# Kernel optimization log

Measured on AMD Instinct MI355X. Metric: run time of the kernel, lower is better.

The kernel has to match this reference:

```python
import math
import jax, jax.numpy as jnp
import numpy as np
from jax import lax

DT = 0.1
IMG_W = 1920.0
IMG_H = 1080.0
DIAG = math.sqrt(IMG_W ** 2 + IMG_H ** 2)


def setup_inputs() -> dict:
    key = jax.random.key(0)
    k1, k2, k3, k4 = jax.random.split(key, 4)
    B, T = 524288, 64
    return {
        "speed": jax.random.uniform(k1, (B, T), dtype=jnp.float32),          # softplus-like, positive
        "yaw_rate": jax.random.normal(k2, (B, T), dtype=jnp.float32) * 0.05,  # rad/step
        "init_pos": jax.random.uniform(k3, (B, 2), dtype=jnp.float32),        # normalized x,y
        "init_heading": jax.random.normal(k4, (B,), dtype=jnp.float32),       # rad
    }


def reference(speed, yaw_rate, init_pos, init_heading):
    B, T = speed.shape
    dtype = speed.dtype
    # per-step yaw decay 0.97**t (the torch loop recomputes this every step; same values)
    decay = jnp.power(jnp.asarray(0.97, dtype), jnp.arange(T, dtype=dtype))
    v_seq = (speed * DIAG).T                      # (T, B) pixel-space speed
    w_seq = (yaw_rate * decay[None, :]).T         # (T, B) decayed yaw rate

    x0 = init_pos[:, 0] * IMG_W
    y0 = init_pos[:, 1] * IMG_H
    psi0 = init_heading

    def step(carry, inp):
        x, y, psi = carry
        v_t, w_t = inp
        is_straight = (jnp.abs(w_t) < 0.01).astype(dtype)
        sin_psi, cos_psi = jnp.sin(psi), jnp.cos(psi)
        dx_straight = v_t * cos_psi * DT
        dy_straight = v_t * sin_psi * DT
        w_safe = w_t + is_straight * 0.0001
        radius = v_t / w_safe
        psi_new = psi + w_t * DT
        dx_turn = radius * (jnp.sin(psi_new) - sin_psi)
        dy_turn = -radius * (jnp.cos(psi_new) - cos_psi)
        dx = is_straight * dx_straight + (1.0 - is_straight) * dx_turn
        dy = is_straight * dy_straight + (1.0 - is_straight) * dy_turn
        x = x + dx
        y = y + dy
        out = jnp.stack([x / IMG_W, y / IMG_H], axis=-1)  # (B, 2)
        return (x, y, psi_new), out

    _, pos = lax.scan(step, (x0, y0, psi0), (v_seq, w_seq))  # pos: (T, B, 2)
    return jnp.transpose(pos, (1, 0, 2))                     # (B, T, 2)
```

## Files before the change

kernel.cpp:

```cpp
#include <hip/hip_runtime.h>
#include <math.h>


#define T_STEPS 64

__global__ __launch_bounds__(256) void kin_scan_kernel(
    const float* __restrict__ speed,
    const float* __restrict__ yaw,
    const float* __restrict__ init_pos,
    const float* __restrict__ init_heading,
    float* __restrict__ out,
    int B)
{
    const float DT    = 0.1f;
    const float IMG_W = 1920.0f;
    const float IMG_H = 1080.0f;
    const float DIAG  = 2202.9071700822459f;
    const float INV_W = 1.0f / 1920.0f;
    const float INV_H = 1.0f / 1080.0f;
    const float LOG2_097 = -0.0439433475875970f;

    const int tid = blockIdx.x * blockDim.x + threadIdx.x;
    const int row = tid >> 4;
    if (row >= B) return;
    const int seg = tid & 15;
    const int t0  = seg * 4;

    const float4* sp4 = reinterpret_cast<const float4*>(speed) + (size_t)row * 16 + seg;
    const float4* yw4 = reinterpret_cast<const float4*>(yaw)   + (size_t)row * 16 + seg;
    float4 v4 = *sp4;
    float4 w4 = *yw4;

    float d  = exp2f((float)t0 * LOG2_097);
    float w0 = w4.x * d; d *= 0.97f;
    float w1 = w4.y * d; d *= 0.97f;
    float w2 = w4.z * d; d *= 0.97f;
    float w3 = w4.w * d;

    float wl = ((w0 + w1) + w2) + w3;
    float s  = wl;
    #pragma unroll
    for (int dlt = 1; dlt < 16; dlt <<= 1) {
        float o = __shfl_up(s, (unsigned)dlt, 16);
        if (seg >= dlt) s += o;
    }
    float wexcl = s - wl;

    const float psi0 = init_heading[row];
    const float2 ip  = reinterpret_cast<const float2*>(init_pos)[row];
    const float x0   = ip.x * IMG_W;
    const float y0   = ip.y * IMG_H;

    float p = psi0 + DT * wexcl;
    float sp, cp;
    sincosf(p, &sp, &cp);

    float dx[4], dy[4];
    float wv[4] = {w0, w1, w2, w3};
    float vv[4] = {v4.x * DIAG, v4.y * DIAG, v4.z * DIAG, v4.w * DIAG};
    #pragma unroll
    for (int j = 0; j < 4; ++j) {
        float v  = vv[j];
        float w  = wv[j];
        float th = w * DT;
        float t2 = th * th;
        float sd  = th * (1.0f + t2 * (-1.666666667e-1f + t2 * 8.333333333e-3f));
        float cm1 = t2 * (-0.5f + t2 * 4.166666667e-2f);
        float ds  = sp * cm1 + cp * sd;
        float dc  = cp * cm1 - sp * sd;
        bool  is_str = fabsf(w) < 0.01f;
        float w_safe = is_str ? (w + 1e-4f) : w;
        float r   = v / w_safe;
        float dxs = v * cp * DT;
        float dys = v * sp * DT;
        float dxt = r * ds;
        float dyt = -r * dc;
        dx[j] = is_str ? dxs : dxt;
        dy[j] = is_str ? dys : dyt;
        sp += ds;
        cp += dc;
    }

    float xi0 = dx[0];
    float xi1 = xi0 + dx[1];
    float xi2 = xi1 + dx[2];
    float xi3 = xi2 + dx[3];
    float yi0 = dy[0];
    float yi1 = yi0 + dy[1];
    float yi2 = yi1 + dy[2];
    float yi3 = yi2 + dy[3];

    float xs = xi3, ys = yi3;
    #pragma unroll
    for (int dlt = 1; dlt < 16; dlt <<= 1) {
        float ox = __shfl_up(xs, (unsigned)dlt, 16);
        float oy = __shfl_up(ys, (unsigned)dlt, 16);
        if (seg >= dlt) { xs += ox; ys += oy; }
    }
    float xb = (xs - xi3) + x0;
    float yb = (ys - yi3) + y0;

    float4 o0, o1;
    o0.x = (xb + xi0) * INV_W;  o0.y = (yb + yi0) * INV_H;
    o0.z = (xb + xi1) * INV_W;  o0.w = (yb + yi1) * INV_H;
    o1.x = (xb + xi2) * INV_W;  o1.y = (yb + yi2) * INV_H;
    o1.z = (xb + xi3) * INV_W;  o1.w = (yb + yi3) * INV_H;

    float4* op = reinterpret_cast<float4*>(out) + (size_t)row * 32 + seg * 2;
    op[0] = o0;
    op[1] = o1;
}

extern "C" void kernel_launch(void* const* d_in, const int* in_sizes, int n_in,
                              void* d_out, int out_size, void* d_ws, size_t ws_size,
                              hipStream_t stream) {
    const float* speed        = (const float*)d_in[0];
    const float* yaw_rate     = (const float*)d_in[1];
    const float* init_pos     = (const float*)d_in[2];
    const float* init_heading = (const float*)d_in[3];
    float* out = (float*)d_out;

    const int B = in_sizes[3];
    const int threads = 256;
    const int total   = B * 16;
    const int blocks  = (total + threads - 1) / threads;

    kin_scan_kernel<<<blocks, threads, 0, stream>>>(
        speed, yaw_rate, init_pos, init_heading, out, B);
}
```

Before: 433.4 us.

## Process eight steps per thread with nontemporal I/O and fast trig intrinsics

Halves threads per row so each thread loads and scans eight timesteps, reducing shuffle stages and raising bytes in flight per thread. Loads and stores use nontemporal builtins to bypass cache retention for streaming data. sincosf and division are replaced with hardware sin/cos (in revolutions) and reciprocal intrinsics, trading some accuracy for fewer instructions.

```diff
diff --git a/kernel.cpp b/kernel.cpp
--- a/kernel.cpp
+++ b/kernel.cpp
@@ -2,7 +2,7 @@
 #include <math.h>
 
 
-#define T_STEPS 64
+using f32x4 = __attribute__((ext_vector_type(4))) float;
 
 __global__ __launch_bounds__(256) void kin_scan_kernel(
     const float* __restrict__ speed,
@@ -19,29 +19,39 @@
     const float INV_W = 1.0f / 1920.0f;
     const float INV_H = 1.0f / 1080.0f;
     const float LOG2_097 = -0.0439433475875970f;
+    const float INV_2PI  = 0.15915494309189535f;
 
     const int tid = blockIdx.x * blockDim.x + threadIdx.x;
-    const int row = tid >> 4;
+    const int row = tid >> 3;
     if (row >= B) return;
-    const int seg = tid & 15;
-    const int t0  = seg * 4;
+    const int seg = tid & 7;
+    const int t0  = seg * 8;
 
-    const float4* sp4 = reinterpret_cast<const float4*>(speed) + (size_t)row * 16 + seg;
-    const float4* yw4 = reinterpret_cast<const float4*>(yaw)   + (size_t)row * 16 + seg;
-    float4 v4 = *sp4;
-    float4 w4 = *yw4;
+    const f32x4* sp4 = reinterpret_cast<const f32x4*>(speed) + (size_t)row * 16 + seg * 2;
+    const f32x4* yw4 = reinterpret_cast<const f32x4*>(yaw)   + (size_t)row * 16 + seg * 2;
+    f32x4 va = __builtin_nontemporal_load(sp4);
+    f32x4 vb = __builtin_nontemporal_load(sp4 + 1);
+    f32x4 wa = __builtin_nontemporal_load(yw4);
+    f32x4 wb = __builtin_nontemporal_load(yw4 + 1);
 
-    float d  = exp2f((float)t0 * LOG2_097);
-    float w0 = w4.x * d; d *= 0.97f;
-    float w1 = w4.y * d; d *= 0.97f;
-    float w2 = w4.z * d; d *= 0.97f;
-    float w3 = w4.w * d;
+    float d = __builtin_amdgcn_exp2f((float)t0 * LOG2_097);
+    float wv[8], vv[8];
+    wv[0] = wa.x * d; d *= 0.97f;
+    wv[1] = wa.y * d; d *= 0.97f;
+    wv[2] = wa.z * d; d *= 0.97f;
+    wv[3] = wa.w * d; d *= 0.97f;
+    wv[4] = wb.x * d; d *= 0.97f;
+    wv[5] = wb.y * d; d *= 0.97f;
+    wv[6] = wb.z * d; d *= 0.97f;
+    wv[7] = wb.w * d;
+    vv[0] = va.x * DIAG; vv[1] = va.y * DIAG; vv[2] = va.z * DIAG; vv[3] = va.w * DIAG;
+    vv[4] = vb.x * DIAG; vv[5] = vb.y * DIAG; vv[6] = vb.z * DIAG; vv[7] = vb.w * DIAG;
 
-    float wl = ((w0 + w1) + w2) + w3;
+    float wl = ((((((wv[0] + wv[1]) + wv[2]) + wv[3]) + wv[4]) + wv[5]) + wv[6]) + wv[7];
     float s  = wl;
     #pragma unroll
-    for (int dlt = 1; dlt < 16; dlt <<= 1) {
-        float o = __shfl_up(s, (unsigned)dlt, 16);
+    for (int dlt = 1; dlt < 8; dlt <<= 1) {
+        float o = __shfl_up(s, (unsigned)dlt, 8);
         if (seg >= dlt) s += o;
     }
     float wexcl = s - wl;
@@ -51,15 +61,15 @@
     const float x0   = ip.x * IMG_W;
     const float y0   = ip.y * IMG_H;
 
-    float p = psi0 + DT * wexcl;
-    float sp, cp;
-    sincosf(p, &sp, &cp);
+    float p   = psi0 + DT * wexcl;
+    float rev = p * INV_2PI;
+    float sp  = __builtin_amdgcn_sinf(rev);
+    float cp  = __builtin_amdgcn_cosf(rev);
 
-    float dx[4], dy[4];
-    float wv[4] = {w0, w1, w2, w3};
-    float vv[4] = {v4.x * DIAG, v4.y * DIAG, v4.z * DIAG, v4.w * DIAG};
+    float xi[8], yi[8];
+    float xacc = 0.0f, yacc = 0.0f;
     #pragma unroll
-    for (int j = 0; j < 4; ++j) {
+    for (int j = 0; j < 8; ++j) {
         float v  = vv[j];
         float w  = wv[j];
         float th = w * DT;
@@ -70,45 +80,34 @@
         float dc  = cp * cm1 - sp * sd;
         bool  is_str = fabsf(w) < 0.01f;
         float w_safe = is_str ? (w + 1e-4f) : w;
-        float r   = v / w_safe;
-        float dxs = v * cp * DT;
-        float dys = v * sp * DT;
-        float dxt = r * ds;
-        float dyt = -r * dc;
-        dx[j] = is_str ? dxs : dxt;
-        dy[j] = is_str ? dys : dyt;
-        sp += ds;
-        cp += dc;
+        float r   = v * __builtin_amdgcn_rcpf(w_safe);
+        float dxv = is_str ? (v * cp * DT) : ( r * ds);
+        float dyv = is_str ? (v * sp * DT) : (-r * dc);
+        xacc += dxv; xi[j] = xacc;
+        yacc += dyv; yi[j] = yacc;
+        sp += ds; cp += dc;
     }
 
-    float xi0 = dx[0];
-    float xi1 = xi0 + dx[1];
-    float xi2 = xi1 + dx[2];
-    float xi3 = xi2 + dx[3];
-    float yi0 = dy[0];
-    float yi1 = yi0 + dy[1];
-    float yi2 = yi1 + dy[2];
-    float yi3 = yi2 + dy[3];
-
-    float xs = xi3, ys = yi3;
+    float xs = xi[7], ys = yi[7];
     #pragma unroll
-    for (int dlt = 1; dlt < 16; dlt <<= 1) {
-        float ox = __shfl_up(xs, (unsigned)dlt, 16);
-        float oy = __shfl_up(ys, (unsigned)dlt, 16);
+    for (int dlt = 1; dlt < 8; dlt <<= 1) {
+        float ox = __shfl_up(xs, (unsigned)dlt, 8);
+        float oy = __shfl_up(ys, (unsigned)dlt, 8);
         if (seg >= dlt) { xs += ox; ys += oy; }
     }
-    float xb = (xs - xi3) + x0;
-    float yb = (ys - yi3) + y0;
+    float xb = (xs - xi[7]) + x0;
+    float yb = (ys - yi[7]) + y0;
 
-    float4 o0, o1;
-    o0.x = (xb + xi0) * INV_W;  o0.y = (yb + yi0) * INV_H;
-    o0.z = (xb + xi1) * INV_W;  o0.w = (yb + yi1) * INV_H;
-    o1.x = (xb + xi2) * INV_W;  o1.y = (yb + yi2) * INV_H;
-    o1.z = (xb + xi3) * INV_W;  o1.w = (yb + yi3) * INV_H;
-
-    float4* op = reinterpret_cast<float4*>(out) + (size_t)row * 32 + seg * 2;
-    op[0] = o0;
-    op[1] = o1;
+    f32x4* op = reinterpret_cast<f32x4*>(out) + (size_t)row * 32 + seg * 4;
+    #pragma unroll
+    for (int k = 0; k < 4; ++k) {
+        f32x4 o;
+        o.x = (xb + xi[2*k    ]) * INV_W;
+        o.y = (yb + yi[2*k    ]) * INV_H;
+        o.z = (xb + xi[2*k + 1]) * INV_W;
+        o.w = (yb + yi[2*k + 1]) * INV_H;
+        __builtin_nontemporal_store(o, op + k);
+    }
 }
 
 extern "C" void kernel_launch(void* const* d_in, const int* in_sizes, int n_in,
@@ -122,7 +121,7 @@
 
     const int B = in_sizes[3];
     const int threads = 256;
-    const int total   = B * 16;
+    const int total   = B * 8;
     const int blocks  = (total + threads - 1) / threads;
 
     kin_scan_kernel<<<blocks, threads, 0, stream>>>(
```

Result: slower. 659.5 us (+52.2%).
